# Kernel tuning notes

Measured on AMD Instinct MI355X. Metric: run time of the kernel, lower is better.

The kernel has to match this reference:

```python
import jax, jax.numpy as jnp
import numpy as np

NX, NC, E = 100000, 50000, 1000000
DIN, DCTX, DH, DOUT = 64, 64, 64, 64


def _linear_params(k, din, dout):
    kw, _ = jax.random.split(k)
    s = 1.0 / np.sqrt(din).astype(np.float32)
    return jax.random.uniform(kw, (dout, din), jnp.float32, -s, s), jnp.zeros((dout,), jnp.float32)


def setup_inputs() -> dict:
    key = jax.random.key(0)
    ks = jax.random.split(key, 16)
    x = jax.random.normal(ks[0], (NX, DIN), jnp.float32)
    c = jax.random.normal(ks[1], (NC, DCTX), jnp.float32)
    e_fwd_src = jax.random.randint(ks[2], (E,), 0, NX, jnp.int32)
    e_fwd_dst = jax.random.randint(ks[3], (E,), 0, NX, jnp.int32)
    e_bwd_src = jax.random.randint(ks[4], (E,), 0, NX, jnp.int32)
    e_bwd_dst = jax.random.randint(ks[5], (E,), 0, NX, jnp.int32)
    e_cx_src = jax.random.randint(ks[6], (E,), 0, NC, jnp.int32)
    e_cx_dst = jax.random.randint(ks[7], (E,), 0, NX, jnp.int32)
    Wx, bx = _linear_params(ks[8], DIN, DH)      # layers['x']
    Wc, bc = _linear_params(ks[9], DCTX, DH)     # layers['c']
    Wff, bff = _linear_params(ks[10], DIN, DH)   # layers['x->x']
    Wbb, bbb = _linear_params(ks[11], DIN, DH)   # layers['x<-x']
    Wcx, bcx = _linear_params(ks[12], DCTX, DH)  # layers['c->x']
    Wp, bp = _linear_params(ks[13], DH, DOUT)    # pool
    return dict(x=x, c=c,
                e_fwd_src=e_fwd_src, e_fwd_dst=e_fwd_dst,
                e_bwd_src=e_bwd_src, e_bwd_dst=e_bwd_dst,
                e_cx_src=e_cx_src, e_cx_dst=e_cx_dst,
                Wx=Wx, bx=bx, Wc=Wc, bc=bc, Wff=Wff, bff=bff,
                Wbb=Wbb, bbb=bbb, Wcx=Wcx, bcx=bcx, Wp=Wp, bp=bp)


def reference(x, c, e_fwd_src, e_fwd_dst, e_bwd_src, e_bwd_dst, e_cx_src, e_cx_dst,
              Wx, bx, Wc, bc, Wff, bff, Wbb, bbb, Wcx, bcx, Wp, bp):
    relu = jax.nn.relu
    seg = lambda v, i: jax.ops.segment_sum(v, i, num_segments=NX)
    # self-loop features
    self_x = relu(x @ Wx.T + bx)                                   # [NX, DH]
    # edge type ('x','->','x'): gather src, transform, scatter-add to dst
    m1 = seg(relu(x[e_fwd_src] @ Wff.T + bff), e_fwd_dst)
    # edge type ('x','<-','x'): direction swap -> true src is stored dst
    m2 = seg(relu(x[e_bwd_dst] @ Wbb.T + bbb), e_bwd_src)
    # edge type ('c','->','x'): gather context nodes
    m3 = seg(relu(c[e_cx_src] @ Wcx.T + bcx), e_cx_dst)
    # coalesce with op='add' over all messages + self loops
    agg = self_x + m1 + m2 + m3                                    # [NX, DH]
    out_x = agg @ Wp.T + bp                                        # [NX, DOUT]
    out_c = relu(c @ Wc.T + bc)                                    # [NC, DH]
    return out_x, out_c
```

## Files before the change

### kernel.cpp

```cpp
#include <hip/hip_runtime.h>
#include <cstddef>

typedef unsigned short ushort_t;
using f32x4  = __attribute__((ext_vector_type(4))) float;
using bf16x8 = __attribute__((ext_vector_type(8))) short;

static constexpr int NX = 100000;
static constexpr int NC = 50000;
static constexpr int E  = 1000000;
static constexpr int E3 = 3 * E;

static constexpr int SHIFT = 6;
static constexpr int BN = 1 << SHIFT;
static constexpr int NB = (NX + BN - 1) / BN;
static constexpr int CAP = 2304;
static constexpr int PF_CHUNK = 4096;
static constexpr int NPF = (E3 + PF_CHUNK - 1) / PF_CHUNK;
static constexpr int NXT = (NX + 63) / 64;
static constexpr int NCT = (NC + 63) / 64;

__device__ inline ushort_t f2bf(float f) {
    unsigned u = __float_as_uint(f);
    return (ushort_t)((u + 0x7fffu + ((u >> 16) & 1u)) >> 16);
}

__device__ inline bf16x8 cvt8(float4 lo, float4 hi) {
    bf16x8 v;
    v[0] = (short)f2bf(lo.x); v[1] = (short)f2bf(lo.y);
    v[2] = (short)f2bf(lo.z); v[3] = (short)f2bf(lo.w);
    v[4] = (short)f2bf(hi.x); v[5] = (short)f2bf(hi.y);
    v[6] = (short)f2bf(hi.z); v[7] = (short)f2bf(hi.w);
    return v;
}

__device__ inline float bfl(unsigned u) { return __uint_as_float(u << 16); }
__device__ inline float bfh(unsigned u) { return __uint_as_float(u & 0xffff0000u); }

__device__ __forceinline__ void gemm_tile(
    const float* __restrict__ in, int nrows, int tile_row0,
    const float* __restrict__ W0, const float* __restrict__ b0, void* __restrict__ o0,
    const float* __restrict__ W1, const float* __restrict__ b1, void* __restrict__ o1,
    const float* __restrict__ W2, const float* __restrict__ b2, void* __restrict__ o2,
    int nlayers, int relu_mask, int bf16_mask)
{
    const int t   = threadIdx.x;
    const int w   = t >> 6;
    const int l   = t & 63;
    const int lr  = l & 15;
    const int lk  = (l >> 4) * 8;
    const int row0 = tile_row0 + (w >> 1) * 32;
    const int col0 = (w & 1) * 32;

    bf16x8 a[2][2];
    #pragma unroll
    for (int m = 0; m < 2; ++m) {
        #pragma unroll
        for (int ks = 0; ks < 2; ++ks) {
            const int row = row0 + 16 * m + lr;
            float4 lo = make_float4(0.f, 0.f, 0.f, 0.f), hi = lo;
            if (row < nrows) {
                const float* p = in + (size_t)row * 64 + ks * 32 + lk;
                lo = *reinterpret_cast<const float4*>(p);
                hi = *reinterpret_cast<const float4*>(p + 4);
            }
            a[m][ks] = cvt8(lo, hi);
        }
    }

    for (int ly = 0; ly < nlayers; ++ly) {
        const float* W = (ly == 0) ? W0 : (ly == 1) ? W1 : W2;
        const float* b = (ly == 0) ? b0 : (ly == 1) ? b1 : b2;
        void*        o = (ly == 0) ? o0 : (ly == 1) ? o1 : o2;

        bf16x8 bf[2][2];
        float  bias[2];
        #pragma unroll
        for (int n = 0; n < 2; ++n) {
            const int col = col0 + 16 * n + lr;
            bias[n] = b[col];
            #pragma unroll
            for (int ks = 0; ks < 2; ++ks) {
                const float* p = W + (size_t)col * 64 + ks * 32 + lk;
                const float4 lo = *reinterpret_cast<const float4*>(p);
                const float4 hi = *reinterpret_cast<const float4*>(p + 4);
                bf[n][ks] = cvt8(lo, hi);
            }
        }

        f32x4 acc[2][2];
        #pragma unroll
        for (int m = 0; m < 2; ++m)
            #pragma unroll
            for (int n = 0; n < 2; ++n)
                acc[m][n] = (f32x4){0.f, 0.f, 0.f, 0.f};

        #pragma unroll
        for (int m = 0; m < 2; ++m) {
            #pragma unroll
            for (int n = 0; n < 2; ++n) {
                acc[m][n] = __builtin_amdgcn_mfma_f32_16x16x32_bf16(a[m][0], bf[n][0], acc[m][n], 0, 0, 0);
                acc[m][n] = __builtin_amdgcn_mfma_f32_16x16x32_bf16(a[m][1], bf[n][1], acc[m][n], 0, 0, 0);
            }
        }

        const bool relu = (relu_mask >> ly) & 1;
        const bool b16  = (bf16_mask >> ly) & 1;
        #pragma unroll
        for (int m = 0; m < 2; ++m) {
            #pragma unroll
            for (int r = 0; r < 4; ++r) {
                const int row = row0 + 16 * m + (l >> 4) * 4 + r;
                if (row < nrows) {
                    #pragma unroll
                    for (int n = 0; n < 2; ++n) {
                        const int col = col0 + 16 * n + lr;
                        float v = acc[m][n][r] + bias[n];
                        if (relu) v = fmaxf(v, 0.f);
                        if (b16) ((ushort_t*)o)[(size_t)row * 64 + col] = f2bf(v);
                        else     ((float*)o)[(size_t)row * 64 + col] = v;
                    }
                }
            }
        }
    }
}

__global__ __launch_bounds__(256) void gemm_partition(
    const float* __restrict__ x, const float* __restrict__ c,
    const float* __restrict__ Wx, const float* __restrict__ bx, ushort_t* __restrict__ h_self,
    const float* __restrict__ Wff, const float* __restrict__ bff, ushort_t* __restrict__ hff,
    const float* __restrict__ Wbb, const float* __restrict__ bbb, ushort_t* __restrict__ hbb,
    const float* __restrict__ Wc, const float* __restrict__ bc, float* __restrict__ out_c,
    const float* __restrict__ Wcx, const float* __restrict__ bcx, ushort_t* __restrict__ hcx,
    const int* __restrict__ efs, const int* __restrict__ efd,
    const int* __restrict__ ebs, const int* __restrict__ ebd,
    const int* __restrict__ ecs, const int* __restrict__ ecd,
    int* __restrict__ bcnt, unsigned* __restrict__ pk)
{
    __shared__ int h[NB];
    __shared__ int base[NB];
    const int b = blockIdx.x;
    if (b >= NPF) {
        const int gb = b - NPF;
        if (gb < NXT)
            gemm_tile(x, NX, gb * 64, Wx, bx, h_self, Wff, bff, hff, Wbb, bbb, hbb, 3, 7, 7);
        else
            gemm_tile(c, NC, (gb - NXT) * 64, Wc, bc, out_c, Wcx, bcx, hcx,
                      nullptr, nullptr, nullptr, 2, 3, 2);
        return;
    }
    for (int i = threadIdx.x; i < NB; i += 256) h[i] = 0;
    __syncthreads();
    const int e0 = b * PF_CHUNK;
    unsigned pack[16];
    int buck[16], rank[16];
    #pragma unroll
    for (int i = 0; i < 16; ++i) {
        const int e = e0 + i * 256 + threadIdx.x;
        buck[i] = -1;
        if (e < E3) {
            int d, sg;
            if (e < E)          { d = efd[e];         sg = efs[e]; }
            else if (e < 2 * E) { d = ebs[e - E];     sg = NX + ebd[e - E]; }
            else                { d = ecd[e - 2 * E]; sg = 2 * NX + ecs[e - 2 * E]; }
            buck[i] = d >> SHIFT;
            pack[i] = ((unsigned)sg << SHIFT) | (unsigned)(d & (BN - 1));
            rank[i] = atomicAdd(&h[buck[i]], 1);
        }
    }
    __syncthreads();
    for (int bb = threadIdx.x; bb < NB; bb += 256)
        base[bb] = h[bb] ? (bb * CAP + atomicAdd(&bcnt[bb], h[bb])) : 0;
    __syncthreads();
    #pragma unroll
    for (int i = 0; i < 16; ++i)
        if (buck[i] >= 0) {
            const int pos = base[buck[i]] + rank[i];
            if (pos < (buck[i] + 1) * CAP)
                pk[pos] = pack[i];
        }
}

__global__ __launch_bounds__(256) void sort_gather_pool(
    const int* __restrict__ bcnt, const unsigned* __restrict__ pk,
    const ushort_t* __restrict__ h_all, const ushort_t* __restrict__ h_self,
    const float* __restrict__ Wp, const float* __restrict__ bp,
    float* __restrict__ out_x)
{
    __shared__ unsigned srt[CAP];
    __shared__ int cnt[BN], nstart[BN], cur[BN];
    __shared__ ushort_t agg_lds[BN * 72];

    const int b = blockIdx.x;
    const int t = threadIdx.x;
    const int s = b * CAP;
    int n = bcnt[b]; if (n > CAP) n = CAP;
    const int tend = s + n;

    if (t < BN) cnt[t] = 0;
    __syncthreads();
    for (int e = s + t; e < tend; e += 256)
        atomicAdd(&cnt[pk[e] & (BN - 1)], 1);
    __syncthreads();
    if (t < BN) {
        const int v = cnt[t];
        int xs = v;
        #pragma unroll
        for (int d = 1; d < BN; d <<= 1) {
            const int y = __shfl_up(xs, d, 64);
            if (t >= d) xs += y;
        }
        nstart[t] = xs - v;
        cur[t]    = xs - v;
    }
    __syncthreads();
    for (int e = s + t; e < tend; e += 256) {
        const unsigned p = pk[e];
        const int pos = atomicAdd(&cur[p & (BN - 1)], 1);
        srt[pos] = (p & ~(unsigned)(BN - 1)) << 1;
    }
    __syncthreads();

    const int w    = t >> 6;
    const int lane = t & 63;
    const int g    = lane >> 3;
    const int fl   = lane & 7;
    const unsigned foff = fl * 16;
    const int node0 = b * BN;
    const char* hb = reinterpret_cast<const char*>(h_all);
    const char* hs = reinterpret_cast<const char*>(h_self);

    for (int i = 0; i < 16; ++i) {
        const int nl   = w * 16 + i;
        const int node = node0 + nl;
        const int start = nstart[nl];
        const int count = cnt[nl];
        float a0 = 0.f, a1 = 0.f, a2 = 0.f, a3 = 0.f;
        float a4 = 0.f, a5 = 0.f, a6 = 0.f, a7 = 0.f;
        if (g == 0 && node < NX) {
            const uint4 u = *reinterpret_cast<const uint4*>(hs + (size_t)node * 128 + foff);
            a0 = bfl(u.x); a1 = bfh(u.x); a2 = bfl(u.y); a3 = bfh(u.y);
            a4 = bfl(u.z); a5 = bfh(u.z); a6 = bfl(u.w); a7 = bfh(u.w);
        }
        int e = g;
        for (; e + 24 < count; e += 32) {
            const unsigned o0 = srt[start + e]      + foff;
            const unsigned o1 = srt[start + e + 8]  + foff;
            const unsigned o2 = srt[start + e + 16] + foff;
            const unsigned o3 = srt[start + e + 24] + foff;
            const uint4 u0 = *reinterpret_cast<const uint4*>(hb + o0);
            const uint4 u1 = *reinterpret_cast<const uint4*>(hb + o1);
            const uint4 u2 = *reinterpret_cast<const uint4*>(hb + o2);
            const uint4 u3 = *reinterpret_cast<const uint4*>(hb + o3);
            a0 += bfl(u0.x) + bfl(u1.x) + bfl(u2.x) + bfl(u3.x);
            a1 += bfh(u0.x) + bfh(u1.x) + bfh(u2.x) + bfh(u3.x);
            a2 += bfl(u0.y) + bfl(u1.y) + bfl(u2.y) + bfl(u3.y);
            a3 += bfh(u0.y) + bfh(u1.y) + bfh(u2.y) + bfh(u3.y);
            a4 += bfl(u0.z) + bfl(u1.z) + bfl(u2.z) + bfl(u3.z);
            a5 += bfh(u0.z) + bfh(u1.z) + bfh(u2.z) + bfh(u3.z);
            a6 += bfl(u0.w) + bfl(u1.w) + bfl(u2.w) + bfl(u3.w);
            a7 += bfh(u0.w) + bfh(u1.w) + bfh(u2.w) + bfh(u3.w);
        }
        for (; e < count; e += 8) {
            const uint4 u = *reinterpret_cast<const uint4*>(hb + (srt[start + e] + foff));
            a0 += bfl(u.x); a1 += bfh(u.x); a2 += bfl(u.y); a3 += bfh(u.y);
            a4 += bfl(u.z); a5 += bfh(u.z); a6 += bfl(u.w); a7 += bfh(u.w);
        }
        a0 += __shfl_xor(a0, 8); a0 += __shfl_xor(a0, 16); a0 += __shfl_xor(a0, 32);
        a1 += __shfl_xor(a1, 8); a1 += __shfl_xor(a1, 16); a1 += __shfl_xor(a1, 32);
        a2 += __shfl_xor(a2, 8); a2 += __shfl_xor(a2, 16); a2 += __shfl_xor(a2, 32);
        a3 += __shfl_xor(a3, 8); a3 += __shfl_xor(a3, 16); a3 += __shfl_xor(a3, 32);
        a4 += __shfl_xor(a4, 8); a4 += __shfl_xor(a4, 16); a4 += __shfl_xor(a4, 32);
        a5 += __shfl_xor(a5, 8); a5 += __shfl_xor(a5, 16); a5 += __shfl_xor(a5, 32);
        a6 += __shfl_xor(a6, 8); a6 += __shfl_xor(a6, 16); a6 += __shfl_xor(a6, 32);
        a7 += __shfl_xor(a7, 8); a7 += __shfl_xor(a7, 16); a7 += __shfl_xor(a7, 32);
        if (lane < 8) {
            uint4 pck;
            pck.x = ((unsigned)f2bf(a1) << 16) | (unsigned)f2bf(a0);
            pck.y = ((unsigned)f2bf(a3) << 16) | (unsigned)f2bf(a2);
            pck.z = ((unsigned)f2bf(a5) << 16) | (unsigned)f2bf(a4);
            pck.w = ((unsigned)f2bf(a7) << 16) | (unsigned)f2bf(a6);
            *reinterpret_cast<uint4*>(&agg_lds[nl * 72 + fl * 8]) = pck;
        }
    }
    __syncthreads();

    const int lr = lane & 15, q4 = lane >> 4;
    const float* wrow = Wp + (size_t)(w * 16 + lr) * 64;
    const bf16x8 bf0 = cvt8(*reinterpret_cast<const float4*>(wrow + q4 * 8),
                            *reinterpret_cast<const float4*>(wrow + q4 * 8 + 4));
    const bf16x8 bf1 = cvt8(*reinterpret_cast<const float4*>(wrow + 32 + q4 * 8),
                            *reinterpret_cast<const float4*>(wrow + 32 + q4 * 8 + 4));
    const float bias = bp[w * 16 + lr];
    #pragma unroll
    for (int rb = 0; rb < 4; ++rb) {
        const bf16x8 af0 = *reinterpret_cast<const bf16x8*>(&agg_lds[(rb * 16 + lr) * 72 + q4 * 8]);
        const bf16x8 af1 = *reinterpret_cast<const bf16x8*>(&agg_lds[(rb * 16 + lr) * 72 + 32 + q4 * 8]);
        f32x4 acc = (f32x4){0.f, 0.f, 0.f, 0.f};
        acc = __builtin_amdgcn_mfma_f32_16x16x32_bf16(af0, bf0, acc, 0, 0, 0);
        acc = __builtin_amdgcn_mfma_f32_16x16x32_bf16(af1, bf1, acc, 0, 0, 0);
        #pragma unroll
        for (int r = 0; r < 4; ++r) {
            const int row = node0 + rb * 16 + q4 * 4 + r;
            if (row < NX)
                out_x[(size_t)row * 64 + w * 16 + lr] = acc[r] + bias;
        }
    }
}

__global__ __launch_bounds__(256) void fused_linear_mfma(
    const float* __restrict__ in, int nrows,
    const float* __restrict__ W0, const float* __restrict__ b0, void* __restrict__ o0,
    const float* __restrict__ W1, const float* __restrict__ b1, void* __restrict__ o1,
    const float* __restrict__ W2, const float* __restrict__ b2, void* __restrict__ o2,
    int nlayers, int relu_mask, int bf16_mask)
{
    gemm_tile(in, nrows, blockIdx.x * 64, W0, b0, o0, W1, b1, o1, W2, b2, o2,
              nlayers, relu_mask, bf16_mask);
}

__global__ __launch_bounds__(256) void scatter_edges(
    const int* __restrict__ efs, const int* __restrict__ efd,
    const int* __restrict__ ebs, const int* __restrict__ ebd,
    const int* __restrict__ ecs, const int* __restrict__ ecd,
    const ushort_t* __restrict__ h_all, float* __restrict__ agg)
{
    const int idx  = blockIdx.x * 256 + threadIdx.x;
    const int lane = idx & 63;
    const int e    = idx >> 6;
    if (e >= E3) return;
    int src, dst;
    if (e < E)          { src = efs[e];           dst = efd[e]; }
    else if (e < 2 * E) { src = NX + ebd[e - E];  dst = ebs[e - E]; }
    else                { src = 2 * NX + ecs[e - 2 * E]; dst = ecd[e - 2 * E]; }
    const unsigned u = (unsigned)h_all[(size_t)src * 64 + lane] << 16;
    atomicAdd(&agg[(size_t)dst * 64 + lane], __uint_as_float(u));
}

extern "C" void kernel_launch(void* const* d_in, const int* in_sizes, int n_in,
                              void* d_out, int out_size, void* d_ws, size_t ws_size,
                              hipStream_t stream)
{
    const float* x   = (const float*)d_in[0];
    const float* c   = (const float*)d_in[1];
    const int*   efs = (const int*)d_in[2];
    const int*   efd = (const int*)d_in[3];
    const int*   ebs = (const int*)d_in[4];
    const int*   ebd = (const int*)d_in[5];
    const int*   ecs = (const int*)d_in[6];
    const int*   ecd = (const int*)d_in[7];
    const float* Wx  = (const float*)d_in[8];
    const float* bx  = (const float*)d_in[9];
    const float* Wc  = (const float*)d_in[10];
    const float* bc  = (const float*)d_in[11];
    const float* Wff = (const float*)d_in[12];
    const float* bff = (const float*)d_in[13];
    const float* Wbb = (const float*)d_in[14];
    const float* bbb = (const float*)d_in[15];
    const float* Wcx = (const float*)d_in[16];
    const float* bcx = (const float*)d_in[17];
    const float* Wp  = (const float*)d_in[18];
    const float* bp  = (const float*)d_in[19];

    float* out_x = (float*)d_out;
    float* out_c = (float*)d_out + (size_t)NX * 64;

    ushort_t* h_all  = (ushort_t*)d_ws;
    ushort_t* hff    = h_all;
    ushort_t* hbb    = h_all + (size_t)NX * 64;
    ushort_t* hcx    = h_all + (size_t)2 * NX * 64;
    ushort_t* h_self = h_all + (size_t)(2 * NX + NC) * 64;
    const size_t h_elems = (size_t)(3 * NX + NC) * 64;

    int* bcnt    = (int*)(h_all + h_elems);
    unsigned* pk = (unsigned*)(bcnt + NB);
    const size_t need_bytes = h_elems * 2 + (size_t)NB * 4 + (size_t)NB * CAP * 4;

    if (ws_size >= need_bytes) {
        hipMemsetAsync(bcnt, 0, (size_t)NB * sizeof(int), stream);
        gemm_partition<<<NPF + NXT + NCT, 256, 0, stream>>>(
            x, c, Wx, bx, h_self, Wff, bff, hff, Wbb, bbb, hbb,
            Wc, bc, out_c, Wcx, bcx, hcx,
            efs, efd, ebs, ebd, ecs, ecd, bcnt, pk);
        sort_gather_pool<<<NB, 256, 0, stream>>>(
            bcnt, pk, h_all, h_self, Wp, bp, out_x);
    } else {
        fused_linear_mfma<<<NXT, 256, 0, stream>>>(
            x, NX, Wx, bx, out_x, Wff, bff, hff, Wbb, bbb, hbb, 3, 7, 6);
        fused_linear_mfma<<<NCT, 256, 0, stream>>>(
            c, NC, Wc, bc, out_c, Wcx, bcx, hcx, nullptr, nullptr, nullptr, 2, 3, 2);
        scatter_edges<<<((size_t)E3 * 64 + 255) / 256, 256, 0, stream>>>(
            efs, efd, ebs, ebd, ecs, ecd, h_all, out_x);
        fused_linear_mfma<<<NXT, 256, 0, stream>>>(
            out_x, NX, Wp, bp, out_x, nullptr, nullptr, nullptr, nullptr, nullptr, nullptr, 1, 0, 0);
    }
}
```

Measured before the change: 147.2 us.

## Use two-pass count-then-scatter partition with larger edge chunks per block

The partition step now takes 16384 edges per block instead of 4096, which cuts the number of global atomicAdds on the per-bucket counters by roughly four times. Because 64 edges per thread no longer fit in registers, the block first reads the destinations to build an LDS histogram. It then reserves global slots and rereads the edges, getting each write position from an LDS atomic on a running cursor. The cost is reading the destination indices twice, fewer partition blocks to overlap with the GEMM tiles, and a placement order within each bucket that is no longer deterministic.

After: 170.7 us. 1.16x slower.

```diff
diff --git a/kernel.cpp b/kernel.cpp
--- a/kernel.cpp
+++ b/kernel.cpp
@@ -14,7 +14,7 @@
 static constexpr int BN = 1 << SHIFT;
 static constexpr int NB = (NX + BN - 1) / BN;
 static constexpr int CAP = 2304;
-static constexpr int PF_CHUNK = 4096;
+static constexpr int PF_CHUNK = 16384;
 static constexpr int NPF = (E3 + PF_CHUNK - 1) / PF_CHUNK;
 static constexpr int NXT = (NX + 63) / 64;
 static constexpr int NCT = (NC + 63) / 64;
@@ -138,7 +138,7 @@
     int* __restrict__ bcnt, unsigned* __restrict__ pk)
 {
     __shared__ int h[NB];
-    __shared__ int base[NB];
+    __shared__ int cur[NB];
     const int b = blockIdx.x;
     if (b >= NPF) {
         const int gb = b - NPF;
@@ -152,33 +152,36 @@
     for (int i = threadIdx.x; i < NB; i += 256) h[i] = 0;
     __syncthreads();
     const int e0 = b * PF_CHUNK;
-    unsigned pack[16];
-    int buck[16], rank[16];
-    #pragma unroll
-    for (int i = 0; i < 16; ++i) {
+
+    #pragma unroll 4
+    for (int i = 0; i < PF_CHUNK / 256; ++i) {
         const int e = e0 + i * 256 + threadIdx.x;
-        buck[i] = -1;
+        if (e < E3) {
+            int d;
+            if (e < E)          d = efd[e];
+            else if (e < 2 * E) d = ebs[e - E];
+            else                d = ecd[e - 2 * E];
+            atomicAdd(&h[d >> SHIFT], 1);
+        }
+    }
+    __syncthreads();
+    for (int bb = threadIdx.x; bb < NB; bb += 256)
+        cur[bb] = h[bb] ? (bb * CAP + atomicAdd(&bcnt[bb], h[bb])) : 0;
+    __syncthreads();
+    #pragma unroll 4
+    for (int i = 0; i < PF_CHUNK / 256; ++i) {
+        const int e = e0 + i * 256 + threadIdx.x;
         if (e < E3) {
             int d, sg;
             if (e < E)          { d = efd[e];         sg = efs[e]; }
             else if (e < 2 * E) { d = ebs[e - E];     sg = NX + ebd[e - E]; }
             else                { d = ecd[e - 2 * E]; sg = 2 * NX + ecs[e - 2 * E]; }
-            buck[i] = d >> SHIFT;
-            pack[i] = ((unsigned)sg << SHIFT) | (unsigned)(d & (BN - 1));
-            rank[i] = atomicAdd(&h[buck[i]], 1);
-        }
-    }
-    __syncthreads();
-    for (int bb = threadIdx.x; bb < NB; bb += 256)
-        base[bb] = h[bb] ? (bb * CAP + atomicAdd(&bcnt[bb], h[bb])) : 0;
-    __syncthreads();
-    #pragma unroll
-    for (int i = 0; i < 16; ++i)
-        if (buck[i] >= 0) {
-            const int pos = base[buck[i]] + rank[i];
-            if (pos < (buck[i] + 1) * CAP)
-                pk[pos] = pack[i];
-        }
+            const int bkt = d >> SHIFT;
+            const int pos = atomicAdd(&cur[bkt], 1);
+            if (pos < (bkt + 1) * CAP)
+                pk[pos] = ((unsigned)sg << SHIFT) | (unsigned)(d & (BN - 1));
+        }
+    }
 }
 
 __global__ __launch_bounds__(256) void sort_gather_pool(
```
